# Performance work log

Hardware: AMD Instinct MI355X
Metric: run time of the kernel (lower is better)

Reference implementation:

```python
import jax, jax.numpy as jnp
import numpy as np

RATE = 0.75
B, L, D = 4, 4096, 1024
NUM_DROP = int(RATE * L)      # 3072
NUM_KEEP = L - NUM_DROP       # 1024


def setup_inputs() -> dict:
    key = jax.random.key(0)
    k1, k2, k3 = jax.random.split(key, 3)
    inputs = jax.random.normal(k1, (B, L, D), dtype=jnp.float32)
    mask_embedding = 0.02 * jax.random.normal(k2, (D,), dtype=jnp.float32)
    # choice without replacement, then sort (as in the module)
    idx_keep = jnp.sort(jax.random.permutation(k3, L)[:NUM_KEEP]).astype(jnp.int32)
    return {"inputs": inputs, "mask_embedding": mask_embedding, "idx_keep": idx_keep}


def reference(inputs, mask_embedding, idx_keep):
    length = inputs.shape[-2]
    iota = jnp.arange(length, dtype=jnp.int32)

    # index_to_mask / mask_to_index
    mask_keep = jnp.zeros((length,), dtype=jnp.int32).at[idx_keep].set(1)
    mask_drop = 1 - mask_keep
    idx_drop = jnp.nonzero(mask_drop, size=NUM_DROP)[0].astype(jnp.int32)

    dt = inputs.dtype
    # SPMD one-hot matmul gather: [num_keep, length] @ [B, length, D]
    onehot_keep = (idx_keep[:, None] == iota[None, :]).astype(dt)
    outputs_dropped = jnp.einsum('kl,bld->bkd', onehot_keep, inputs)

    # SPMD one-hot matmul scatter of the broadcast mask embedding
    me = mask_embedding.astype(dt)
    updates = jnp.tile(me, (NUM_DROP, 1))                      # [num_drop, D]
    onehot_drop = (idx_drop[:, None] == iota[None, :]).astype(dt)
    scattered = jnp.einsum('nl,nd->ld', onehot_drop, updates)  # [length, D]
    outputs_masked = inputs * mask_keep.astype(dt)[:, None] + scattered

    return (outputs_dropped, outputs_masked, mask_drop.astype(jnp.float32), idx_keep)
```

## Files before the change

### kernel.cpp

```cpp
#include <hip/hip_runtime.h>


#define B_ 4
#define L_ 4096
#define D_ 1024
#define NKEEP_ 1024
#define ROWS_PER_BLOCK 8

__global__ __launch_bounds__(256) void masktoken_kernel(
    const float4* __restrict__ in,
    const float4* __restrict__ me,
    const int4*   __restrict__ idx_keep4,
    float4* __restrict__ out0,
    float4* __restrict__ out1,
    float*  __restrict__ out2,
    float*  __restrict__ out3)
{
    const int t = threadIdx.x;

    __shared__ int srank[L_];

    const int4   kv = idx_keep4[t];
    const float4 mv = me[t];

    #pragma unroll
    for (int i = 0; i < L_ / 256; ++i) srank[t + 256 * i] = -1;
    __syncthreads();
    srank[kv.x] = 4 * t + 0;
    srank[kv.y] = 4 * t + 1;
    srank[kv.z] = 4 * t + 2;
    srank[kv.w] = 4 * t + 3;
    __syncthreads();

    const int row0 = blockIdx.x * ROWS_PER_BLOCK;

    #pragma unroll
    for (int i = 0; i < ROWS_PER_BLOCK; ++i) {
        const int row = row0 + i;
        const int b   = row >> 12;
        const int l   = row & (L_ - 1);

        const int r = srank[l];

        const size_t rowOff = (size_t)row * (D_ / 4);
        if (r >= 0) {
            float4 v = in[rowOff + t];
            out1[rowOff + t] = v;
            out0[((size_t)b * NKEEP_ + (size_t)r) * (D_ / 4) + t] = v;
        } else {
            out1[rowOff + t] = mv;
        }

        if (b == 0 && t == 0) {
            out2[l] = (r < 0) ? 1.0f : 0.0f;
            if (r >= 0) out3[r] = (float)l;
        }
    }
}

extern "C" void kernel_launch(void* const* d_in, const int* in_sizes, int n_in,
                              void* d_out, int out_size, void* d_ws, size_t ws_size,
                              hipStream_t stream) {
    const float4* in  = (const float4*)d_in[0];
    const float4* me  = (const float4*)d_in[1];
    const int4*   idx = (const int4*)d_in[2];

    float* out = (float*)d_out;
    float4* out0 = (float4*)out;
    float4* out1 = (float4*)(out + (size_t)B_ * NKEEP_ * D_);
    float*  out2 = out + (size_t)B_ * NKEEP_ * D_ + (size_t)B_ * L_ * D_;
    float*  out3 = out2 + L_;

    dim3 grid(B_ * L_ / ROWS_PER_BLOCK);
    dim3 block(256);
    masktoken_kernel<<<grid, block, 0, stream>>>(in, me, idx, out0, out1, out2, out3);
}
```

Before: 131.5 us.

## Replace shared-memory rank table with per-wave linear search and ballot

Each block previously built a 4096-entry shared-memory rank table with two barriers before processing 8 rows. Now each block handles one sequence position across two batches, and every wave scans all 1024 keep indices (4 int4 loads per lane), then uses a ballot and shuffle to find that position's rank. This removes the shared-memory initialisation and the barriers, but each block redundantly reads the whole index array (L2-resident) and launches 8192 smaller blocks with less work per block.

After: 128.1 us. 1.03x faster.

```diff
diff --git a/kernel.cpp b/kernel.cpp
--- a/kernel.cpp
+++ b/kernel.cpp
@@ -5,7 +5,6 @@
 #define L_ 4096
 #define D_ 1024
 #define NKEEP_ 1024
-#define ROWS_PER_BLOCK 8
 
 __global__ __launch_bounds__(256) void masktoken_kernel(
     const float4* __restrict__ in,
@@ -16,33 +15,33 @@
     float*  __restrict__ out2,
     float*  __restrict__ out3)
 {
-    const int t = threadIdx.x;
+    const int q    = blockIdx.x;
+    const int l    = q & (L_ - 1);
+    const int bp   = q >> 12;
+    const int t    = threadIdx.x;
+    const int lane = t & 63;
 
-    __shared__ int srank[L_];
-
-    const int4   kv = idx_keep4[t];
     const float4 mv = me[t];
 
+    int m = -1;
     #pragma unroll
-    for (int i = 0; i < L_ / 256; ++i) srank[t + 256 * i] = -1;
-    __syncthreads();
-    srank[kv.x] = 4 * t + 0;
-    srank[kv.y] = 4 * t + 1;
-    srank[kv.z] = 4 * t + 2;
-    srank[kv.w] = 4 * t + 3;
-    __syncthreads();
+    for (int j = 0; j < 4; ++j) {
+        const int  k4 = lane + 64 * j;
+        const int4 kv = idx_keep4[k4];
+        const int  kb = 4 * k4;
+        if (kv.x == l) m = kb + 0;
+        if (kv.y == l) m = kb + 1;
+        if (kv.z == l) m = kb + 2;
+        if (kv.w == l) m = kb + 3;
+    }
+    const unsigned long long bal = __ballot(m >= 0);
+    const int r = bal ? __shfl(m, __ffsll((long long)bal) - 1) : -1;
 
-    const int row0 = blockIdx.x * ROWS_PER_BLOCK;
-
+    const int b0 = bp << 1;
     #pragma unroll
-    for (int i = 0; i < ROWS_PER_BLOCK; ++i) {
-        const int row = row0 + i;
-        const int b   = row >> 12;
-        const int l   = row & (L_ - 1);
-
-        const int r = srank[l];
-
-        const size_t rowOff = (size_t)row * (D_ / 4);
+    for (int bb = 0; bb < 2; ++bb) {
+        const int b = b0 + bb;
+        const size_t rowOff = (size_t)(b * L_ + l) * (D_ / 4);
         if (r >= 0) {
             float4 v = in[rowOff + t];
             out1[rowOff + t] = v;
@@ -50,11 +49,11 @@
         } else {
             out1[rowOff + t] = mv;
         }
+    }
 
-        if (b == 0 && t == 0) {
-            out2[l] = (r < 0) ? 1.0f : 0.0f;
-            if (r >= 0) out3[r] = (float)l;
-        }
+    if (bp == 0 && t == 0) {
+        out2[l] = (r < 0) ? 1.0f : 0.0f;
+        if (r >= 0) out3[r] = (float)l;
     }
 }
 
@@ -71,7 +70,7 @@
     float*  out2 = out + (size_t)B_ * NKEEP_ * D_ + (size_t)B_ * L_ * D_;
     float*  out3 = out2 + L_;
 
-    dim3 grid(B_ * L_ / ROWS_PER_BLOCK);
+    dim3 grid(2 * L_);
     dim3 block(256);
     masktoken_kernel<<<grid, block, 0, stream>>>(in, me, idx, out0, out1, out2, out3);
 }
```
